# Kernel tuning notes

Measured on AMD Instinct MI355X. Metric: run time of the kernel, lower is better.

Reference implementation:

```python
import jax, jax.numpy as jnp
import numpy as np

NUM_BBOX = 2
NUM_CLASSES = 20
NUM_GRID = 7
THR_CONF = 0.5
THR_NMS = 0.3
BATCH = 128


def setup_inputs() -> dict:
    key = jax.random.key(0)
    C = NUM_BBOX * 4 + NUM_BBOX + NUM_CLASSES  # 30
    p = jax.random.normal(key, (BATCH, NUM_GRID, NUM_GRID, C), dtype=jnp.float32)
    return {"p_yolo_ts4": p}


def _decode(p):
    B, S = p.shape[0], p.shape[1]
    sc = NUM_BBOX * 4
    conf = jax.nn.sigmoid(p[..., sc:sc + NUM_BBOX])          # [B,S,S,nb] objectness
    cls = jax.nn.sigmoid(p[..., sc + NUM_BBOX:])             # [B,S,S,nc]
    boxes = p[..., :sc].reshape(B, S, S, NUM_BBOX, 4)
    xy = jax.nn.sigmoid(boxes[..., :2])                      # cell-relative offsets
    col = jnp.arange(S, dtype=p.dtype)
    cx = (xy[..., 0] + col[None, None, :, None]) / NUM_GRID  # + col index (x)
    cy = (xy[..., 1] + col[None, :, None, None]) / NUM_GRID  # + row index (y)
    w, h = boxes[..., 2], boxes[..., 3]                      # raw wh, as in source
    ltrb = jnp.stack([cx - w / 2, cy - h / 2, cx + w / 2, cy + h / 2], axis=-1)
    labels = jnp.argmax(cls, axis=-1) + 1                    # [B,S,S]
    valid = conf > THR_CONF                                  # [B,S,S,nb]
    return ltrb, conf, labels, valid


def _pairwise_iou(b):
    lt = jnp.maximum(b[:, None, :2], b[None, :, :2])
    rb = jnp.minimum(b[:, None, 2:], b[None, :, 2:])
    wh = jnp.clip(rb - lt, 0.0)
    inter = wh[..., 0] * wh[..., 1]
    area = (b[:, 2] - b[:, 0]) * (b[:, 3] - b[:, 1])
    union = area[:, None] + area[None, :] - inter
    return inter / jnp.maximum(union, 1e-9)


def reference(p_yolo_ts4):
    p = p_yolo_ts4
    B, S = p.shape[0], p.shape[1]
    ltrb, conf, labels, valid = _decode(p)
    N = B * S * S * NUM_BBOX
    boxes = ltrb.reshape(N, 4)
    scores = conf.reshape(N)
    labs = jnp.broadcast_to(labels[..., None], (B, S, S, NUM_BBOX)).reshape(N)
    idsb = jnp.broadcast_to(jnp.arange(B)[:, None, None, None], (B, S, S, NUM_BBOX)).reshape(N)
    vmask = valid.reshape(N)
    # sort by score (invalid last); greedy NMS per (batch, label) group
    order = jnp.argsort(jnp.where(vmask, scores, -jnp.inf))[::-1]
    boxes_s = boxes[order]
    scores_s = scores[order]
    labs_s = labs[order]
    idsb_s = idsb[order]
    v_s = vmask[order]
    iou = _pairwise_iou(boxes_s)                              # [N,N]
    same = (idsb_s[:, None] == idsb_s[None, :]) & (labs_s[:, None] == labs_s[None, :])
    later = jnp.arange(N)[None, :] > jnp.arange(N)[:, None]
    sup_mat = (iou > THR_NMS) & same & later & v_s[None, :]

    def body(i, sup):
        keep_i = v_s[i] & jnp.logical_not(sup[i])
        return jnp.where(keep_i, sup | sup_mat[i], sup)

    sup = jax.lax.fori_loop(0, N, body, jnp.zeros((N,), dtype=bool))
    keep = v_s & jnp.logical_not(sup)
    # fixed-shape outputs in descending-score order; `keep` marks surviving boxes
    return idsb_s, boxes_s, labs_s, scores_s, keep
```

## Files before the change

kernel.cpp:

```cpp
#include <hip/hip_runtime.h>
#include <math.h>

#define NBATCH 128
#define S 7
#define CH 30
#define N 12544
#define PERB 98
#define NWORDS 196
#define NCHUNK 16
#define CLENMAX 784
#define POISON 0xAAAAAAAAu
#define THRNMS 0.3

__device__ __forceinline__ float sigf(float x) {
    float e = (float)exp(-(double)x);
    return 1.0f / (1.0f + e);
}

__global__ __launch_bounds__(256) void k_decode(
    const float* __restrict__ p,
    float4* __restrict__ box4,
    float* __restrict__ score,
    int* __restrict__ meta,
    unsigned long long* __restrict__ ballots,
    unsigned long long* __restrict__ vK,
    unsigned int* __restrict__ vrank,
    unsigned int* __restrict__ counter)
{
    int i    = blockIdx.x * 256 + threadIdx.x;
    int lane = threadIdx.x & 63;
    int j    = i & 1;
    int cell = i >> 1;
    int x = cell % S, y = (cell / S) % S;
    const float* pc = p + cell * CH;

    float tx = pc[j*4+0], ty = pc[j*4+1], tw = pc[j*4+2], th = pc[j*4+3];
    float craw = pc[8 + j];

    int cbase = 10 + j * 10;
    float best = pc[cbase]; int lab = j * 10;
    #pragma unroll
    for (int c = 1; c < 10; ++c) {
        float v = pc[cbase + c];
        if (v > best) { best = v; lab = j * 10 + c; }
    }
    float obest = __shfl_xor(best, 1);
    int   olab  = __shfl_xor(lab, 1);
    float bestA = j ? obest : best;  int labA = j ? olab : lab;
    float bestB = j ? best  : obest; int labB = j ? lab  : olab;
    int label = (bestB > bestA ? labB : labA) + 1;

    float sx = sigf(tx), sy = sigf(ty);
    float cx = (sx + (float)x) / 7.0f;
    float cy = (sy + (float)y) / 7.0f;
    float hw = tw / 2.0f, hh = th / 2.0f;
    float l = cx - hw, t = cy - hh, r = cx + hw, bt = cy + hh;

    float sc = sigf(craw);
    bool valid = sc > 0.5f;

    box4[i]  = make_float4(l, t, r, bt);
    score[i] = sc;
    meta[i]  = label;

    unsigned long long vb = __ballot(valid);
    if (lane == 0) ballots[i >> 6] = vb;

    unsigned int wcnt = (unsigned int)__popcll(vb);
    unsigned int basec = 0;
    if (lane == 0 && wcnt) basec = atomicAdd(counter, wcnt);
    basec = __shfl(basec, 0);
    if (valid) {
        unsigned int slot = (basec - POISON)
                          + (unsigned int)__popcll(vb & ((1ull << lane) - 1ull));
        vK[slot] = ((unsigned long long)__float_as_uint(sc) << 32)
                   | (unsigned long long)(unsigned int)i;
        vrank[slot] = 0u;
    }
}

__global__ __launch_bounds__(256) void k_rankv(
    const unsigned long long* __restrict__ vK,
    const unsigned int* __restrict__ counter,
    unsigned int* __restrict__ vrank)
{
    __shared__ unsigned long long lk[CLENMAX];
    const unsigned int nv = counter[0] - POISON;
    if ((unsigned int)(blockIdx.x * 256) >= nv) return;
    unsigned int clen = (nv + NCHUNK - 1) / NCHUNK;
    unsigned int base = blockIdx.y * clen;
    if (base >= nv) return;
    unsigned int len = (nv - base < clen) ? nv - base : clen;

    for (unsigned int u = threadIdx.x; u < len; u += 256) lk[u] = vK[base + u];
    __syncthreads();

    unsigned int s = blockIdx.x * 256 + threadIdx.x;
    if (s < nv) {
        unsigned long long Ki = vK[s];
        unsigned int cnt = 0;
        for (unsigned int u = 0; u < len; ++u)
            cnt += (lk[u] > Ki) ? 1u : 0u;
        if (cnt) atomicAdd(&vrank[s], cnt);
    }
}

__global__ __launch_bounds__(256) void k_finish(
    const unsigned long long* __restrict__ vK,
    const unsigned int* __restrict__ counter,
    const unsigned int* __restrict__ vrank,
    const unsigned long long* __restrict__ ballots,
    const float4* __restrict__ box4,
    const float* __restrict__ score,
    const int* __restrict__ meta,
    float* __restrict__ out)
{
    const int b   = blockIdx.x;
    const int tid = threadIdx.x;
    __shared__ unsigned long long blds[NWORDS];
    __shared__ unsigned long long mK[PERB];
    __shared__ int mslot[PERB];
    __shared__ unsigned int cnt_sh;
    __shared__ float sbx[PERB][4];
    __shared__ int   slb[PERB], spos[PERB], sup[PERB];
    __shared__ float ssc[PERB];

    if (tid == 0) cnt_sh = 0u;
    if (tid < NWORDS) blds[tid] = ballots[tid];
    __syncthreads();

    const unsigned int nv = counter[0] - POISON;
    for (unsigned int s = tid; s < nv; s += 256) {
        unsigned long long K = vK[s];
        unsigned int idx = (unsigned int)(K & 0xFFFFFFFFull);
        if ((int)(idx / PERB) == b) {
            unsigned int m = atomicAdd(&cnt_sh, 1u);
            mK[m] = K; mslot[m] = (int)s;
        }
    }
    __syncthreads();
    const int kb = (int)cnt_sh;

    if (tid < kb) {
        unsigned long long Kt = mK[tid];
        int rk = 0;
        for (int u = 0; u < kb; ++u) rk += (mK[u] > Kt) ? 1 : 0;
        unsigned int idx = (unsigned int)(Kt & 0xFFFFFFFFull);
        float4 b4 = box4[idx];
        sbx[rk][0] = b4.x; sbx[rk][1] = b4.y; sbx[rk][2] = b4.z; sbx[rk][3] = b4.w;
        slb[rk]  = meta[idx];
        ssc[rk]  = score[idx];
        spos[rk] = (int)vrank[mslot[tid]];
        sup[rk]  = 0;
    }
    __syncthreads();

    for (int i = 0; i < kb; ++i) {
        __syncthreads();
        if (sup[i]) continue;
        float li = sbx[i][0], ti = sbx[i][1], ri = sbx[i][2], bi = sbx[i][3];
        float areai = (ri - li) * (bi - ti);
        int labi = slb[i];
        int jj = tid;
        if (jj > i && jj < kb && slb[jj] == labi) {
            float lj = sbx[jj][0], tj = sbx[jj][1], rj = sbx[jj][2], bj = sbx[jj][3];
            float lt0 = fmaxf(li, lj), lt1 = fmaxf(ti, tj);
            float rb0 = fminf(ri, rj), rb1 = fminf(bi, bj);
            float w = rb0 - lt0; if (w < 0.0f) w = 0.0f;
            float h = rb1 - lt1; if (h < 0.0f) h = 0.0f;
            float inter = w * h;
            float areaj = (rj - lj) * (bj - tj);
            float uni = areai + areaj - inter;
            double iou = (double)inter / fmax((double)uni, 1e-9);
            if (iou > THRNMS) sup[jj] = 1;
        }
    }
    __syncthreads();

    if (tid < kb) {
        int pos = spos[tid];
        out[pos] = (float)b;
        ((float4*)(out + N))[pos] =
            make_float4(sbx[tid][0], sbx[tid][1], sbx[tid][2], sbx[tid][3]);
        out[5*N + pos] = (float)slb[tid];
        out[6*N + pos] = ssc[tid];
        out[7*N + pos] = sup[tid] ? 0.0f : 1.0f;
    }

    if (tid < PERB) {
        int i = b * PERB + tid;
        bool validown = (blds[i >> 6] >> (i & 63)) & 1ull;
        if (!validown) {
            unsigned int vle = 0;
            int wmax = i >> 6;
            for (int w = 0; w < wmax; ++w) vle += (unsigned int)__popcll(blds[w]);
            vle += (unsigned int)__popcll(blds[wmax] & ((1ull << (i & 63)) - 1ull));
            unsigned int pos = (unsigned int)(N - 1 - i) + vle;
            out[pos] = (float)b;
            ((float4*)(out + N))[pos] = box4[i];
            out[5*N + pos] = (float)meta[i];
            out[6*N + pos] = score[i];
            out[7*N + pos] = 0.0f;
        }
    }
}

extern "C" void kernel_launch(void* const* d_in, const int* in_sizes, int n_in,
                              void* d_out, int out_size, void* d_ws, size_t ws_size,
                              hipStream_t stream)
{
    const float* p = (const float*)d_in[0];
    float* out = (float*)d_out;

    char* w = (char*)d_ws;
    float4* box4          = (float4*)w;               w += (size_t)N * 16;
    unsigned long long* vK = (unsigned long long*)w;  w += (size_t)N * 8;
    unsigned long long* ballots = (unsigned long long*)w; w += (size_t)NWORDS * 8;
    float* score          = (float*)w;                w += (size_t)N * 4;
    int* meta             = (int*)w;                  w += (size_t)N * 4;
    unsigned int* vrank   = (unsigned int*)w;         w += (size_t)N * 4;
    unsigned int* counter = (unsigned int*)w;         w += 4;

    k_decode<<<dim3(N / 256),    dim3(256), 0, stream>>>(p, box4, score, meta,
                                                         ballots, vK, vrank, counter);
    k_rankv <<<dim3(49, NCHUNK), dim3(256), 0, stream>>>(vK, counter, vrank);
    k_finish<<<dim3(NBATCH),     dim3(256), 0, stream>>>(vK, counter, vrank, ballots,
                                                         box4, score, meta, out);
}
```

Baseline: 85.19 us.

## Rank all boxes with one packed key instead of compacting valid boxes

Removes the atomic compaction of valid boxes and the ballot-based placement of invalid ones. Every box now gets a 64-bit key holding its score (zero when invalid), its index and its label, and a single full pairwise ranking pass gives every output position. The finish kernel reads its batch's boxes directly, needs no global scan over the compacted list, and drops to 128 threads. In exchange the ranking kernel always compares all N keys rather than only the valid ones, which is about double the work when roughly half the boxes are valid.

Measured after the change: 86.49 us. Within noise of the previous version (+1.5%).

```diff
diff --git a/kernel.cpp b/kernel.cpp
--- a/kernel.cpp
+++ b/kernel.cpp
@@ -6,10 +6,8 @@
 #define CH 30
 #define N 12544
 #define PERB 98
-#define NWORDS 196
 #define NCHUNK 16
-#define CLENMAX 784
-#define POISON 0xAAAAAAAAu
+#define CLEN 784
 #define THRNMS 0.3
 
 __device__ __forceinline__ float sigf(float x) {
@@ -21,14 +19,10 @@
     const float* __restrict__ p,
     float4* __restrict__ box4,
     float* __restrict__ score,
-    int* __restrict__ meta,
-    unsigned long long* __restrict__ ballots,
     unsigned long long* __restrict__ vK,
-    unsigned int* __restrict__ vrank,
-    unsigned int* __restrict__ counter)
+    unsigned int* __restrict__ vrank)
 {
     int i    = blockIdx.x * 256 + threadIdx.x;
-    int lane = threadIdx.x & 63;
     int j    = i & 1;
     int cell = i >> 1;
     int x = cell % S, y = (cell / S) % S;
@@ -61,97 +55,85 @@
 
     box4[i]  = make_float4(l, t, r, bt);
     score[i] = sc;
-    meta[i]  = label;
 
-    unsigned long long vb = __ballot(valid);
-    if (lane == 0) ballots[i >> 6] = vb;
-
-    unsigned int wcnt = (unsigned int)__popcll(vb);
-    unsigned int basec = 0;
-    if (lane == 0 && wcnt) basec = atomicAdd(counter, wcnt);
-    basec = __shfl(basec, 0);
-    if (valid) {
-        unsigned int slot = (basec - POISON)
-                          + (unsigned int)__popcll(vb & ((1ull << lane) - 1ull));
-        vK[slot] = ((unsigned long long)__float_as_uint(sc) << 32)
-                   | (unsigned long long)(unsigned int)i;
-        vrank[slot] = 0u;
-    }
+    unsigned long long lowk = ((unsigned long long)(unsigned int)i << 7)
+                            | (unsigned long long)(unsigned int)label;
+    vK[i] = valid ? ((unsigned long long)__float_as_uint(sc) << 32) | lowk
+                  : lowk;
+    vrank[i] = 0u;
 }
 
 __global__ __launch_bounds__(256) void k_rankv(
     const unsigned long long* __restrict__ vK,
-    const unsigned int* __restrict__ counter,
     unsigned int* __restrict__ vrank)
 {
-    __shared__ unsigned long long lk[CLENMAX];
-    const unsigned int nv = counter[0] - POISON;
-    if ((unsigned int)(blockIdx.x * 256) >= nv) return;
-    unsigned int clen = (nv + NCHUNK - 1) / NCHUNK;
-    unsigned int base = blockIdx.y * clen;
-    if (base >= nv) return;
-    unsigned int len = (nv - base < clen) ? nv - base : clen;
-
-    for (unsigned int u = threadIdx.x; u < len; u += 256) lk[u] = vK[base + u];
+    __shared__ unsigned long long lk[CLEN];
+    const unsigned int base = blockIdx.y * CLEN;
+    for (unsigned int u = threadIdx.x; u < CLEN; u += 256)
+        lk[u] = vK[base + u];
     __syncthreads();
 
-    unsigned int s = blockIdx.x * 256 + threadIdx.x;
-    if (s < nv) {
-        unsigned long long Ki = vK[s];
-        unsigned int cnt = 0;
-        for (unsigned int u = 0; u < len; ++u)
-            cnt += (lk[u] > Ki) ? 1u : 0u;
-        if (cnt) atomicAdd(&vrank[s], cnt);
-    }
+    const unsigned int s = blockIdx.x * 256 + threadIdx.x;
+    const unsigned long long Ki = vK[s];
+    unsigned int cnt = 0;
+    #pragma unroll 16
+    for (unsigned int u = 0; u < CLEN; ++u)
+        cnt += (lk[u] > Ki) ? 1u : 0u;
+    if (cnt) atomicAdd(&vrank[s], cnt);
 }
 
-__global__ __launch_bounds__(256) void k_finish(
+__global__ __launch_bounds__(128) void k_finish(
     const unsigned long long* __restrict__ vK,
-    const unsigned int* __restrict__ counter,
     const unsigned int* __restrict__ vrank,
-    const unsigned long long* __restrict__ ballots,
     const float4* __restrict__ box4,
     const float* __restrict__ score,
-    const int* __restrict__ meta,
     float* __restrict__ out)
 {
     const int b   = blockIdx.x;
     const int tid = threadIdx.x;
-    __shared__ unsigned long long blds[NWORDS];
     __shared__ unsigned long long mK[PERB];
-    __shared__ int mslot[PERB];
-    __shared__ unsigned int cnt_sh;
     __shared__ float sbx[PERB][4];
     __shared__ int   slb[PERB], spos[PERB], sup[PERB];
     __shared__ float ssc[PERB];
+    __shared__ unsigned int wcnt[2];
 
-    if (tid == 0) cnt_sh = 0u;
-    if (tid < NWORDS) blds[tid] = ballots[tid];
+    const int gi = b * PERB + tid;
+    bool isv = false;
+    unsigned long long K = 0ull;
+    unsigned int r = 0u;
+    float sc = 0.0f;
+    float4 b4 = make_float4(0.f, 0.f, 0.f, 0.f);
+    if (tid < PERB) {
+        K  = vK[gi];
+        r  = vrank[gi];
+        sc = score[gi];
+        b4 = box4[gi];
+        isv = (K >> 32) != 0ull;
+        mK[tid] = K;
+    }
+    unsigned long long vb = __ballot(isv);
+    if ((tid & 63) == 0) wcnt[tid >> 6] = (unsigned int)__popcll(vb);
     __syncthreads();
+    const int kb = (int)(wcnt[0] + wcnt[1]);
 
-    const unsigned int nv = counter[0] - POISON;
-    for (unsigned int s = tid; s < nv; s += 256) {
-        unsigned long long K = vK[s];
-        unsigned int idx = (unsigned int)(K & 0xFFFFFFFFull);
-        if ((int)(idx / PERB) == b) {
-            unsigned int m = atomicAdd(&cnt_sh, 1u);
-            mK[m] = K; mslot[m] = (int)s;
+    if (tid < PERB) {
+        int label = (int)(K & 0x7Full);
+        if (isv) {
+            int rk = 0;
+            #pragma unroll
+            for (int u = 0; u < PERB; ++u) rk += (mK[u] > K) ? 1 : 0;
+            sbx[rk][0] = b4.x; sbx[rk][1] = b4.y; sbx[rk][2] = b4.z; sbx[rk][3] = b4.w;
+            slb[rk]  = label;
+            ssc[rk]  = sc;
+            spos[rk] = (int)r;
+            sup[rk]  = 0;
+        } else {
+            out[r] = (float)b;
+            ((float4*)(out + N))[r] = b4;
+            out[5*N + r] = (float)label;
+            out[6*N + r] = sc;
+            out[7*N + r] = 0.0f;
         }
-    }
-    __syncthreads();
-    const int kb = (int)cnt_sh;
-
-    if (tid < kb) {
-        unsigned long long Kt = mK[tid];
-        int rk = 0;
-        for (int u = 0; u < kb; ++u) rk += (mK[u] > Kt) ? 1 : 0;
-        unsigned int idx = (unsigned int)(Kt & 0xFFFFFFFFull);
-        float4 b4 = box4[idx];
-        sbx[rk][0] = b4.x; sbx[rk][1] = b4.y; sbx[rk][2] = b4.z; sbx[rk][3] = b4.w;
-        slb[rk]  = meta[idx];
-        ssc[rk]  = score[idx];
-        spos[rk] = (int)vrank[mslot[tid]];
-        sup[rk]  = 0;
     }
     __syncthreads();
 
@@ -186,23 +168,6 @@
         out[6*N + pos] = ssc[tid];
         out[7*N + pos] = sup[tid] ? 0.0f : 1.0f;
     }
-
-    if (tid < PERB) {
-        int i = b * PERB + tid;
-        bool validown = (blds[i >> 6] >> (i & 63)) & 1ull;
-        if (!validown) {
-            unsigned int vle = 0;
-            int wmax = i >> 6;
-            for (int w = 0; w < wmax; ++w) vle += (unsigned int)__popcll(blds[w]);
-            vle += (unsigned int)__popcll(blds[wmax] & ((1ull << (i & 63)) - 1ull));
-            unsigned int pos = (unsigned int)(N - 1 - i) + vle;
-            out[pos] = (float)b;
-            ((float4*)(out + N))[pos] = box4[i];
-            out[5*N + pos] = (float)meta[i];
-            out[6*N + pos] = score[i];
-            out[7*N + pos] = 0.0f;
-        }
-    }
 }
 
 extern "C" void kernel_launch(void* const* d_in, const int* in_sizes, int n_in,
@@ -213,17 +178,12 @@
     float* out = (float*)d_out;
 
     char* w = (char*)d_ws;
-    float4* box4          = (float4*)w;               w += (size_t)N * 16;
+    float4* box4           = (float4*)w;              w += (size_t)N * 16;
     unsigned long long* vK = (unsigned long long*)w;  w += (size_t)N * 8;
-    unsigned long long* ballots = (unsigned long long*)w; w += (size_t)NWORDS * 8;
-    float* score          = (float*)w;                w += (size_t)N * 4;
-    int* meta             = (int*)w;                  w += (size_t)N * 4;
-    unsigned int* vrank   = (unsigned int*)w;         w += (size_t)N * 4;
-    unsigned int* counter = (unsigned int*)w;         w += 4;
+    float* score           = (float*)w;               w += (size_t)N * 4;
+    unsigned int* vrank    = (unsigned int*)w;        w += (size_t)N * 4;
 
-    k_decode<<<dim3(N / 256),    dim3(256), 0, stream>>>(p, box4, score, meta,
-                                                         ballots, vK, vrank, counter);
-    k_rankv <<<dim3(49, NCHUNK), dim3(256), 0, stream>>>(vK, counter, vrank);
-    k_finish<<<dim3(NBATCH),     dim3(256), 0, stream>>>(vK, counter, vrank, ballots,
-                                                         box4, score, meta, out);
+    k_decode<<<dim3(N / 256),       dim3(256), 0, stream>>>(p, box4, score, vK, vrank);
+    k_rankv <<<dim3(49, NCHUNK),    dim3(256), 0, stream>>>(vK, vrank);
+    k_finish<<<dim3(NBATCH),        dim3(128), 0, stream>>>(vK, vrank, box4, score, out);
 }
```
